# Kernel tuning notes

Hardware: AMD Instinct MI355X
Metric: run time of the kernel (lower is better)

## Reference

```python
import jax, jax.numpy as jnp
import numpy as np


def _log_g(x):
    # numerically stable log of g(x) = where(x>=0, x+0.5, sigmoid(x))
    return jnp.where(x >= 0, jnp.log(jax.nn.relu(x) + 0.5), -jax.nn.softplus(-x))


def setup_inputs() -> dict:
    key = jax.random.key(0)
    k1, k2, k3, k4 = jax.random.split(key, 4)
    B, T, D = 4, 4096, 1024
    Di = 2 * D  # dim_inner = int(dim * expansion_factor), expansion_factor = 2.0
    x = jax.random.normal(k1, (B, T, D), dtype=jnp.float32)
    prev_hidden = jax.random.uniform(k2, (B, Di), dtype=jnp.float32)  # positive carry state
    # torch Linear(dim, 2*dim_inner, bias=False): stored here pre-transposed as [D, 2*Di]
    W_hg = jax.random.normal(k3, (D, 2 * Di), dtype=jnp.float32) * (1.0 / np.sqrt(D))
    # out_proj Linear(dim_inner, dim, bias=False): stored pre-transposed as [Di, D]
    W_out = jax.random.normal(k4, (Di, D), dtype=jnp.float32) * (1.0 / np.sqrt(Di))
    return {"x": x, "prev_hidden": prev_hidden, "W_hg": W_hg, "W_out": W_out}


def reference(x, prev_hidden, W_hg, W_out):
    # x: [B, T, D]; prev_hidden: [B, Di] (positive)
    T = x.shape[1]
    hg = jnp.einsum('btd,de->bte', x, W_hg)          # [B, T, 2*Di]
    hidden, gate = jnp.split(hg, 2, axis=-1)          # each [B, T, Di]

    # Heinsen log-space affine scan: h_t = (1 - z_t) * h_{t-1} + z_t * g(hidden_t)
    log_coeffs = -jax.nn.softplus(gate)               # log(1 - sigmoid(gate))
    log_values = -jax.nn.softplus(-gate) + _log_g(hidden)  # log(sigmoid(gate)) + log g(hidden)

    # prepend carry state
    prev_log = jnp.clip(jnp.log(jnp.clip(prev_hidden, 1e-8, None)), -30.0, None)[:, None]  # [B,1,Di]
    log_values = jnp.concatenate([prev_log, log_values], axis=1)      # [B, T+1, Di]
    log_coeffs = jnp.pad(log_coeffs, ((0, 0), (1, 0), (0, 0)))        # [B, T+1, Di]

    a_star = jnp.cumsum(log_coeffs, axis=1)
    h = jnp.exp(a_star + jax.lax.cumlogsumexp(log_values - a_star, axis=1))  # [B, T+1, Di]
    h = h[:, -T:]                                     # drop carry slot

    next_hidden = h[:, -1]                            # [B, Di]
    out = jnp.einsum('bte,ed->btd', h, W_out)         # [B, T, D]
    return (out, next_hidden)
```

## Files before the change

### kernel.cpp

```cpp
#include <hip/hip_runtime.h>
#include <cstdio>

#define T_LEN 4096
#define B_SZ  4
#define D_IN  1024
#define DI    2048
#define MM    16384
#define NC    32
#define CHL   128

typedef __attribute__((ext_vector_type(8))) __bf16 bf16x8;
typedef __attribute__((ext_vector_type(4))) float  f32x4;
typedef __attribute__((ext_vector_type(8))) unsigned short u16x8;

__device__ __forceinline__ unsigned short f2bf(float f){
  unsigned u = __builtin_bit_cast(unsigned, f);
  u += 0x7fffu + ((u >> 16) & 1u);
  return (unsigned short)(u >> 16);
}
__device__ __forceinline__ float bf2f_lo(unsigned u){
  return __builtin_bit_cast(float, u << 16);
}
__device__ __forceinline__ float bf2f_hi(unsigned u){
  return __builtin_bit_cast(float, u & 0xffff0000u);
}

__device__ __forceinline__ void async16(void* lds, const void* g){
  __builtin_amdgcn_global_load_lds((const __attribute__((address_space(1))) void*)g,
                                   (__attribute__((address_space(3))) void*)lds, 16, 0, 0);
}

__global__ __launch_bounds__(256) void k_convert_x(const float* __restrict__ x,
                                                   unsigned short* __restrict__ xb){
  size_t t = (size_t)blockIdx.x*256 + threadIdx.x;
  const float4* xi = (const float4*)x;
  float4 a = xi[2*t], b = xi[2*t+1];
  u16x8 o;
  o[0]=f2bf(a.x); o[1]=f2bf(a.y); o[2]=f2bf(a.z); o[3]=f2bf(a.w);
  o[4]=f2bf(b.x); o[5]=f2bf(b.y); o[6]=f2bf(b.z); o[7]=f2bf(b.w);
  ((u16x8*)xb)[t] = o;
}

template<int PERM>
__global__ __launch_bounds__(256) void k_transpose(const float* __restrict__ src,
                                                   unsigned short* __restrict__ dst,
                                                   int SK, int SN){
  __shared__ float tile[64][65];
  int n0 = blockIdx.x*64, k0 = blockIdx.y*64;
  #pragma unroll
  for(int it=0; it<16; it++){
    int idx = it*256 + threadIdx.x;
    int kk = idx>>6, nn = idx&63;
    int n = n0+nn;
    int col = PERM ? (((n>>5)<<4) + (n&15) + ((n&16)?2048:0)) : n;
    tile[kk][nn] = src[(size_t)(k0+kk)*SN + col];
  }
  __syncthreads();
  #pragma unroll
  for(int it=0; it<16; it++){
    int idx = it*256 + threadIdx.x;
    int nn = idx>>6, kk = idx&63;
    dst[(size_t)(n0+nn)*SK + k0+kk] = f2bf(tile[kk][nn]);
  }
}

template<int EPI>
__global__ __launch_bounds__(256, 2)
void k_gemm(const unsigned short* __restrict__ A, const unsigned short* __restrict__ Bt,
            float* __restrict__ C0, unsigned short* __restrict__ U0,
            unsigned short* __restrict__ U1, float* __restrict__ Ap,
            float* __restrict__ Vp, int M, int N, int K){
  __shared__ unsigned short lsA[128*32];
  __shared__ unsigned short lsB[128*32];
  int tid  = threadIdx.x;
  int lane = tid & 63, wave = tid >> 6;
  int wm = wave >> 1, wn = wave & 1;
  int cl = lane & 15, quad = lane >> 4;
  int m0 = blockIdx.y * 128, n0 = blockIdx.x * 128;

  f32x4 acc[4][4];
  #pragma unroll
  for(int i=0;i<4;i++)
    #pragma unroll
    for(int j=0;j<4;j++) acc[i][j] = (f32x4){0.f,0.f,0.f,0.f};

  int cs = (tid&3) ^ ((tid>>3)&3);
  const unsigned short* gA = A  + (size_t)(m0 + (tid>>2))*K + cs*8;
  const unsigned short* gB = Bt + (size_t)(n0 + (tid>>2))*K + cs*8;
  unsigned short* dA = lsA + tid*8;
  unsigned short* dB = lsB + tid*8;
  int qa8 = (quad ^ ((cl>>1)&3)) * 8;

  for(int k0=0; k0<K; k0+=32){
    async16(dA,        gA + k0);
    async16(dA + 2048, gA + (size_t)64*K + k0);
    async16(dB,        gB + k0);
    async16(dB + 2048, gB + (size_t)64*K + k0);
    __syncthreads();
    bf16x8 fa[4], fb[4];
    #pragma unroll
    for(int t2=0;t2<4;t2++){
      fa[t2] = *(const bf16x8*)&lsA[(wm*64 + t2*16 + cl)*32 + qa8];
      fb[t2] = *(const bf16x8*)&lsB[(wn*64 + t2*16 + cl)*32 + qa8];
    }
    #pragma unroll
    for(int i=0;i<4;i++)
      #pragma unroll
      for(int j=0;j<4;j++)
        acc[i][j] = __builtin_amdgcn_mfma_f32_16x16x32_bf16(fa[i], fb[j], acc[i][j], 0, 0, 0);
    __syncthreads();
  }

  if(EPI==0){
    #pragma unroll
    for(int i=0;i<4;i++)
      #pragma unroll
      for(int j=0;j<4;j++){
        int n = n0 + wn*64 + j*16 + cl;
        #pragma unroll
        for(int r=0;r<4;r++){
          int m = m0 + wm*64 + i*16 + quad*4 + r;
          C0[(size_t)m*N + n] = acc[i][j][r];
        }
      }
  } else {
    float* lA_f = (float*)lsA;
    float* lV_f = (float*)lsB;
    int ibase = ((n0 + wn*64) >> 1) + cl;
    #pragma unroll
    for(int i=0;i<4;i++)
      #pragma unroll
      for(int p=0;p<2;p++){
        f32x4 hh = acc[i][2*p], gg = acc[i][2*p+1];
        int ii = ibase + p*16;
        float pa = 1.f, pv = 0.f;
        #pragma unroll
        for(int r=0;r<4;r++){
          int m = m0 + wm*64 + i*16 + quad*4 + r;
          float gate = gg[r], hid = hh[r];
          float e  = __expf(gate);
          float cc = 1.f/(1.f + e);
          float z  = (gate > 80.f) ? 1.f : e*cc;
          float gv = (hid >= 0.f) ? (hid + 0.5f) : (1.f/(1.f + __expf(-hid)));
          float vv = z*gv;
          U0[(size_t)m*DI + ii] = f2bf(cc);
          U1[(size_t)m*DI + ii] = f2bf(vv);
          pa *= cc;
          pv = fmaf(cc, pv, vv);
        }
        int seg = wm*16 + i*4 + quad;
        int chl = wn*32 + p*16 + cl;
        lA_f[seg*64 + chl] = pa;
        lV_f[seg*64 + chl] = pv;
      }
    __syncthreads();
    if(tid < 64){
      float Ac = 1.f, Vc = 0.f;
      #pragma unroll 8
      for(int s=0; s<32; s++){
        float a = lA_f[s*64 + tid], v = lV_f[s*64 + tid];
        Ac *= a;
        Vc = fmaf(a, Vc, v);
      }
      size_t o = (size_t)(m0 >> 7)*DI + (n0 >> 1) + tid;
      Ap[o] = Ac; Vp[o] = Vc;
    }
  }
}

__global__ __launch_bounds__(256) void k_scanB(const float* __restrict__ prev,
                                               const float* __restrict__ Ap,
                                               const float* __restrict__ Vp,
                                               float* __restrict__ hin){
  int t = blockIdx.x*256 + threadIdx.x;
  int i = t & (DI-1); int b = t >> 11;
  float h = fmaxf(prev[t], 1e-8f);
  for(int ch=0; ch<NC; ch++){
    size_t o = (size_t)(b*NC + ch)*DI + i;
    hin[o] = h;
    h = fmaf(Ap[o], h, Vp[o]);
  }
}

__global__ __launch_bounds__(256) void k_scanC(const unsigned* __restrict__ cp,
                                               unsigned* __restrict__ vp,
                                               const float* __restrict__ hin,
                                               float* __restrict__ nh){
  int t = blockIdx.x*256 + threadIdx.x;
  int i2 = t & (DI/2 - 1);
  int ch = (t >> 10) & (NC-1);
  int b  = t >> 15;
  size_t base = ((size_t)(b*T_LEN + ch*CHL))*(DI/2) + i2;
  size_t ho = (size_t)(b*NC + ch)*DI + 2*i2;
  float h0 = hin[ho], h1 = hin[ho+1];
  #pragma unroll 4
  for(int s=0; s<CHL; s++){
    unsigned cu = cp[base], vu = vp[base];
    h0 = fmaf(bf2f_lo(cu), h0, bf2f_lo(vu));
    h1 = fmaf(bf2f_hi(cu), h1, bf2f_hi(vu));
    vp[base] = (unsigned)f2bf(h0) | ((unsigned)f2bf(h1) << 16);
    base += DI/2;
  }
  if(ch == NC-1){ nh[b*DI + 2*i2] = h0; nh[b*DI + 2*i2 + 1] = h1; }
}

extern "C" void kernel_launch(void* const* d_in, const int* in_sizes, int n_in,
                              void* d_out, int out_size, void* d_ws, size_t ws_size,
                              hipStream_t stream){
  const float* x    = (const float*)d_in[0];
  const float* prev = (const float*)d_in[1];
  const float* Whg  = (const float*)d_in[2];
  const float* Wout = (const float*)d_in[3];
  float* out = (float*)d_out;
  float* nh  = out + (size_t)MM*D_IN;

  const size_t NEED = 116391936;
  if(ws_size < NEED){
    fprintf(stderr, "kernel_launch: ws_size=%zu < needed %zu — aborting launch\n",
            ws_size, NEED);
    return;
  }
  char* ws = (char*)d_ws;
  unsigned short* xb = (unsigned short*)(ws);
  unsigned short* wt = (unsigned short*)(ws + 33554432);
  unsigned short* wo = (unsigned short*)(ws + 41943040);
  unsigned short* v  = (unsigned short*)(ws + 46137344);
  float* Ap  = (float*)(ws + 113246208);
  float* Vp  = (float*)(ws + 114294784);
  float* hin = (float*)(ws + 115343360);
  unsigned short* c = (unsigned short*)d_out;

  k_convert_x<<<8192, 256, 0, stream>>>(x, xb);
  k_transpose<1><<<dim3(64,16), 256, 0, stream>>>(Whg,  wt, 1024, 4096);
  k_transpose<0><<<dim3(16,32), 256, 0, stream>>>(Wout, wo, 2048, 1024);

  k_gemm<1><<<dim3(32,128), 256, 0, stream>>>(xb, wt, nullptr, c, v, Ap, Vp,
                                              MM, 2*DI, D_IN);

  k_scanB<<<32,  256, 0, stream>>>(prev, Ap, Vp, hin);
  k_scanC<<<512, 256, 0, stream>>>((const unsigned*)c, (unsigned*)v, hin, nh);

  k_gemm<0><<<dim3(8,128), 256, 0, stream>>>(v, wo, out, nullptr, nullptr,
                                             nullptr, nullptr, MM, D_IN, DI);
}
```

Before: 424.7 us.

## Fuse prep kernels into one launch and halve scan chunk length

The three preprocessing kernels (x conversion plus two weight transposes) become a single launch that dispatches by block index. The chunked scan now uses 64 chunks of 64 steps instead of 32 of 128. The GEMM epilogue emits two partial aggregates per tile, and the scan-C launch doubles in size, which shortens the serial dependency chain and raises parallelism. scanB writes the carry-in values back over Ap in place, so the separate hin buffer is no longer used, at the cost of a serial scanB loop twice as long.

```diff
diff --git a/kernel.cpp b/kernel.cpp
--- a/kernel.cpp
+++ b/kernel.cpp
@@ -6,8 +6,8 @@
 #define D_IN  1024
 #define DI    2048
 #define MM    16384
-#define NC    32
-#define CHL   128
+#define NC2   64
+#define CHL2  64
 
 typedef __attribute__((ext_vector_type(8))) __bf16 bf16x8;
 typedef __attribute__((ext_vector_type(4))) float  f32x4;
@@ -30,26 +30,14 @@
                                    (__attribute__((address_space(3))) void*)lds, 16, 0, 0);
 }
 
-__global__ __launch_bounds__(256) void k_convert_x(const float* __restrict__ x,
-                                                   unsigned short* __restrict__ xb){
-  size_t t = (size_t)blockIdx.x*256 + threadIdx.x;
-  const float4* xi = (const float4*)x;
-  float4 a = xi[2*t], b = xi[2*t+1];
-  u16x8 o;
-  o[0]=f2bf(a.x); o[1]=f2bf(a.y); o[2]=f2bf(a.z); o[3]=f2bf(a.w);
-  o[4]=f2bf(b.x); o[5]=f2bf(b.y); o[6]=f2bf(b.z); o[7]=f2bf(b.w);
-  ((u16x8*)xb)[t] = o;
-}
-
 template<int PERM>
-__global__ __launch_bounds__(256) void k_transpose(const float* __restrict__ src,
-                                                   unsigned short* __restrict__ dst,
-                                                   int SK, int SN){
-  __shared__ float tile[64][65];
-  int n0 = blockIdx.x*64, k0 = blockIdx.y*64;
+__device__ __forceinline__ void transpose_body(const float* __restrict__ src,
+                                               unsigned short* __restrict__ dst,
+                                               int n0, int k0, int SK, int SN,
+                                               float (*tile)[65], int tid){
   #pragma unroll
   for(int it=0; it<16; it++){
-    int idx = it*256 + threadIdx.x;
+    int idx = it*256 + tid;
     int kk = idx>>6, nn = idx&63;
     int n = n0+nn;
     int col = PERM ? (((n>>5)<<4) + (n&15) + ((n&16)?2048:0)) : n;
@@ -58,9 +46,34 @@
   __syncthreads();
   #pragma unroll
   for(int it=0; it<16; it++){
-    int idx = it*256 + threadIdx.x;
+    int idx = it*256 + tid;
     int nn = idx>>6, kk = idx&63;
     dst[(size_t)(n0+nn)*SK + k0+kk] = f2bf(tile[kk][nn]);
+  }
+}
+
+__global__ __launch_bounds__(256) void k_prep(const float* __restrict__ x,
+                                              unsigned short* __restrict__ xb,
+                                              const float* __restrict__ Whg,
+                                              unsigned short* __restrict__ wt,
+                                              const float* __restrict__ Wout,
+                                              unsigned short* __restrict__ wo){
+  __shared__ float tile[64][65];
+  int bid = blockIdx.x, tid = threadIdx.x;
+  if(bid < 8192){
+    size_t t = (size_t)bid*256 + tid;
+    const float4* xi = (const float4*)x;
+    float4 a = xi[2*t], b = xi[2*t+1];
+    u16x8 o;
+    o[0]=f2bf(a.x); o[1]=f2bf(a.y); o[2]=f2bf(a.z); o[3]=f2bf(a.w);
+    o[4]=f2bf(b.x); o[5]=f2bf(b.y); o[6]=f2bf(b.z); o[7]=f2bf(b.w);
+    ((u16x8*)xb)[t] = o;
+  } else if(bid < 9216){
+    int j = bid - 8192;
+    transpose_body<1>(Whg, wt, (j&63)*64, (j>>6)*64, 1024, 4096, tile, tid);
+  } else {
+    int j = bid - 9216;
+    transpose_body<0>(Wout, wo, (j&15)*64, (j>>4)*64, 2048, 1024, tile, tid);
   }
 }
 
@@ -154,31 +167,35 @@
         lV_f[seg*64 + chl] = pv;
       }
     __syncthreads();
-    if(tid < 64){
+    if(tid < 128){
+      int ch = tid & 63, q = tid >> 6;
       float Ac = 1.f, Vc = 0.f;
       #pragma unroll 8
-      for(int s=0; s<32; s++){
-        float a = lA_f[s*64 + tid], v = lV_f[s*64 + tid];
+      for(int s=0; s<16; s++){
+        int idx = (q*16 + s)*64 + ch;
+        float a = lA_f[idx], v = lV_f[idx];
         Ac *= a;
         Vc = fmaf(a, Vc, v);
       }
-      size_t o = (size_t)(m0 >> 7)*DI + (n0 >> 1) + tid;
+      int b = m0 >> 12;
+      int ch64 = ((m0 & 4095) >> 6) + q;
+      size_t o = (size_t)(b*NC2 + ch64)*DI + (n0 >> 1) + ch;
       Ap[o] = Ac; Vp[o] = Vc;
     }
   }
 }
 
 __global__ __launch_bounds__(256) void k_scanB(const float* __restrict__ prev,
-                                               const float* __restrict__ Ap,
-                                               const float* __restrict__ Vp,
-                                               float* __restrict__ hin){
+                                               float* __restrict__ Ap,
+                                               const float* __restrict__ Vp){
   int t = blockIdx.x*256 + threadIdx.x;
   int i = t & (DI-1); int b = t >> 11;
   float h = fmaxf(prev[t], 1e-8f);
-  for(int ch=0; ch<NC; ch++){
-    size_t o = (size_t)(b*NC + ch)*DI + i;
-    hin[o] = h;
-    h = fmaf(Ap[o], h, Vp[o]);
+  for(int ch=0; ch<NC2; ch++){
+    size_t o = (size_t)(b*NC2 + ch)*DI + i;
+    float a = Ap[o], vv = Vp[o];
+    Ap[o] = h;
+    h = fmaf(a, h, vv);
   }
 }
 
@@ -188,20 +205,21 @@
                                                float* __restrict__ nh){
   int t = blockIdx.x*256 + threadIdx.x;
   int i2 = t & (DI/2 - 1);
-  int ch = (t >> 10) & (NC-1);
-  int b  = t >> 15;
-  size_t base = ((size_t)(b*T_LEN + ch*CHL))*(DI/2) + i2;
-  size_t ho = (size_t)(b*NC + ch)*DI + 2*i2;
-  float h0 = hin[ho], h1 = hin[ho+1];
+  int ch = (t >> 10) & (NC2-1);
+  int b  = t >> 16;
+  size_t base = ((size_t)(b*T_LEN + ch*CHL2))*(DI/2) + i2;
+  const float2* hin2 = (const float2*)hin;
+  float2 h01 = hin2[(size_t)(b*NC2 + ch)*(DI/2) + i2];
+  float h0 = h01.x, h1 = h01.y;
   #pragma unroll 4
-  for(int s=0; s<CHL; s++){
+  for(int s=0; s<CHL2; s++){
     unsigned cu = cp[base], vu = vp[base];
     h0 = fmaf(bf2f_lo(cu), h0, bf2f_lo(vu));
     h1 = fmaf(bf2f_hi(cu), h1, bf2f_hi(vu));
     vp[base] = (unsigned)f2bf(h0) | ((unsigned)f2bf(h1) << 16);
     base += DI/2;
   }
-  if(ch == NC-1){ nh[b*DI + 2*i2] = h0; nh[b*DI + 2*i2 + 1] = h1; }
+  if(ch == NC2-1){ nh[b*DI + 2*i2] = h0; nh[b*DI + 2*i2 + 1] = h1; }
 }
 
 extern "C" void kernel_launch(void* const* d_in, const int* in_sizes, int n_in,
@@ -214,7 +232,7 @@
   float* out = (float*)d_out;
   float* nh  = out + (size_t)MM*D_IN;
 
-  const size_t NEED = 116391936;
+  const size_t NEED = 117440512;
   if(ws_size < NEED){
     fprintf(stderr, "kernel_launch: ws_size=%zu < needed %zu — aborting launch\n",
             ws_size, NEED);
@@ -226,19 +244,16 @@
   unsigned short* wo = (unsigned short*)(ws + 41943040);
   unsigned short* v  = (unsigned short*)(ws + 46137344);
   float* Ap  = (float*)(ws + 113246208);
-  float* Vp  = (float*)(ws + 114294784);
-  float* hin = (float*)(ws + 115343360);
+  float* Vp  = (float*)(ws + 115343360);
   unsigned short* c = (unsigned short*)d_out;
 
-  k_convert_x<<<8192, 256, 0, stream>>>(x, xb);
-  k_transpose<1><<<dim3(64,16), 256, 0, stream>>>(Whg,  wt, 1024, 4096);
-  k_transpose<0><<<dim3(16,32), 256, 0, stream>>>(Wout, wo, 2048, 1024);
+  k_prep<<<9728, 256, 0, stream>>>(x, xb, Whg, wt, Wout, wo);
 
   k_gemm<1><<<dim3(32,128), 256, 0, stream>>>(xb, wt, nullptr, c, v, Ap, Vp,
                                               MM, 2*DI, D_IN);
 
-  k_scanB<<<32,  256, 0, stream>>>(prev, Ap, Vp, hin);
-  k_scanC<<<512, 256, 0, stream>>>((const unsigned*)c, (unsigned*)v, hin, nh);
+  k_scanB<<<32,   256, 0, stream>>>(prev, Ap, Vp);
+  k_scanC<<<1024, 256, 0, stream>>>((const unsigned*)c, (unsigned*)v, Ap, nh);
 
   k_gemm<0><<<dim3(8,128), 256, 0, stream>>>(v, wo, out, nullptr, nullptr,
                                              nullptr, nullptr, MM, D_IN, DI);
```

After: 424.6 us. About the same (-0.0%).
